# Optimization experiments

Measured on AMD Instinct MI355X. Metric: run time of the kernel, lower is better.

Reference implementation:

```python
import jax, jax.numpy as jnp
import numpy as np

B, L, P = 65536, 512, 96
E_LIN, E = 14, 16
FFT = 512
TEMP = 0.07
K = 2
EPS = 1e-5


def setup_inputs() -> dict:
    key = jax.random.key(0)
    k0, k1, k2 = jax.random.split(key, 3)
    x = jax.random.normal(k0, (B, L), dtype=jnp.float32)
    Wg = jax.random.normal(k1, (E, FFT // 2), dtype=jnp.float32) * 0.02
    bg = jnp.zeros((E,), dtype=jnp.float32)
    Wr = jax.random.normal(k2, (E_LIN, P, L), dtype=jnp.float32) * 0.02
    br = jnp.zeros((E_LIN, P), dtype=jnp.float32)
    return {"x": x, "Wg": Wg, "bg": bg, "Wr": Wr, "br": br}


def _periodogram(x):
    # x: [B, L] -> normalized power spectrum [B, FFT//2]
    x0 = x - jnp.mean(x, axis=1, keepdims=True)
    dft = jnp.fft.fft(x0, n=FFT, axis=1) / np.float32(np.sqrt(FFT))
    dft = dft[:, : FFT // 2]
    I = dft.real ** 2 + dft.imag ** 2
    s = jnp.sum(I, axis=1, keepdims=True)
    s = jnp.where(s == 0, jnp.ones_like(s), s)
    return I / s


def reference(x, Wg, bg, Wr, br):
    # gating (eval mode: no noise, divide by temperature)
    I = _periodogram(x)                                  # [B, F/2]
    gate = (I @ Wg.T + bg) / TEMP                        # [B, E]
    topv, topi = jax.lax.top_k(gate, K)                  # [B, K]
    gates = jax.nn.softmax(topv, axis=1)                 # [B, K]

    # RLinear experts: RevIN(norm) -> Linear -> RevIN(denorm); stats detached
    mu = jax.lax.stop_gradient(jnp.mean(x, axis=1, keepdims=True))        # [B,1]
    sd = jax.lax.stop_gradient(jnp.sqrt(jnp.var(x, axis=1, keepdims=True) + EPS))
    xn = (x - mu) / sd                                   # [B, L]
    yr = jnp.einsum('bl,epl->bep', xn, Wr) + br          # [B, E_LIN, P]
    yr = yr * sd[:, :, None] + mu[:, :, None]

    mean_out = jnp.broadcast_to(jnp.mean(x, axis=1, keepdims=True), (x.shape[0], P))[:, None, :]
    naive_out = jnp.broadcast_to(x[:, -1:], (x.shape[0], P))[:, None, :]

    eo = jnp.concatenate([yr, mean_out, naive_out], axis=1)   # [B, E, P]
    sel = jnp.take_along_axis(eo, topi[:, :, None], axis=1)   # [B, K, P]
    out = jnp.sum(gates[:, :, None] * sel, axis=1)            # [B, P]
    return out
```

## Files before the change

kernel.cpp:

```cpp
#include <hip/hip_runtime.h>
#include <math.h>

#define NB_B 65536
#define NL   512
#define NP   96
#define NE   16
#define NEL  14
#define NF   256
#define TEMP_INV (1.0f/0.07f)
#define TAU  1e-5f
#define PI_D 3.14159265358979323846
#define MAXCHK 1280

typedef __attribute__((ext_vector_type(8))) short bf16x8;
typedef __attribute__((ext_vector_type(4))) float f32x4;


#define WS_PCNT     0
#define WS_PTK      16384
#define WS_PBASE    32768
#define WS_FLAGCNT  33792
#define WS_NCHK     33824
#define WS_FLAG     33856
#define WS_SSUM     296000
#define WS_WGT      301376
#define WS_BGT      317760
#define WS_TWF      317824
#define WS_TWD      319872
#define WS_REC      328064
#define WS_HDR      590208
#define WS_RIDX     1638784
#define WS_WRB      1900928
#define WS_DESC     3473792
#define WS_XB16     3480064

__device__ __forceinline__ unsigned short f2bf(float f) {
    unsigned u = __float_as_uint(f);
    unsigned r = (u + 0x7fffu + ((u >> 16) & 1u)) >> 16;
    return (unsigned short)r;
}

__global__ __launch_bounds__(256) void k_prep(
    const float* __restrict__ Wg, const float* __restrict__ bg,
    const float* __restrict__ Wr,
    float* __restrict__ Ssum, float* __restrict__ WgE, float* __restrict__ bgT,
    double2* __restrict__ twd,
    int* __restrict__ pcnt, int* __restrict__ flagcnt,
    ushort4* __restrict__ Wrb, int perm)
{
    int g = blockIdx.x * 256 + threadIdx.x;
    {
        ushort4 o = make_ushort4(0, 0, 0, 0);
        if (g < NEL * NP * NL / 4) {
            float4 v;
            if (perm) {
                int row = g >> 7, sq = g & 127;
                int ll = sq >> 1, kb = (sq & 1) * 4;
                const float* wr = Wr + (size_t)row * NL + ll;
                v.x = wr[(kb + 0) * 64]; v.y = wr[(kb + 1) * 64];
                v.z = wr[(kb + 2) * 64]; v.w = wr[(kb + 3) * 64];
            } else {
                v = ((const float4*)Wr)[g];
            }
            o.x = f2bf(v.x); o.y = f2bf(v.y); o.z = f2bf(v.z); o.w = f2bf(v.w);
        }
        Wrb[g] = o;
    }
    if (g < NEL * NP) {
        const float4* w = (const float4*)(Wr + (size_t)g * NL);
        float s = 0.f;
        for (int i = 0; i < NL / 4; i++) { float4 v = w[i]; s += v.x + v.y + v.z + v.w; }
        Ssum[g] = s;
    }
    if (g < 4096) {
        int c = g & 3, e = (g >> 2) & 15, f4 = g >> 6;
        WgE[g] = Wg[e * NF + f4 * 4 + c] * TEMP_INV;
    }
    if (g < 512) {
        double a = -2.0 * PI_D * (double)g / 512.0;
        twd[g] = make_double2(cos(a), sin(a));
    }
    if (g < 256) pcnt[g << 4] = 0;
    if (g < NE) bgT[g] = bg[g] * TEMP_INV;
    if (g == 300) *flagcnt = 0;
}

__global__ __launch_bounds__(256) void k_gate(
    const float* __restrict__ x,
    const float4* __restrict__ WgE4, const float* __restrict__ bgT,
    int* __restrict__ rec, float4* __restrict__ hdr,
    int* __restrict__ flaglist, int* __restrict__ flagcnt,
    int* __restrict__ pcnt, unsigned short* __restrict__ xb16)
{
    __shared__ __align__(16) float2 s_z[4][576];
    float* s_Iv = (float*)&s_z[0][0];

    const int t = threadIdx.x;
    const int wv = t >> 6, l = t & 63;
    const int b0 = blockIdx.x * 8 + wv * 2;

    const float kAng = -6.283185307179586f / 512.0f;
    auto mktw = [&](int g) {
        float s_, c_;
        __sincosf((float)g * kAng, &s_, &c_);
        return make_float2(c_, s_);
    };
    float2 tw0[4], tw1[2];
#pragma unroll
    for (int k = 0; k < 4; k++) tw0[k] = mktw(k * 64 + l);
    tw1[0] = mktw(2 * l);
    tw1[1] = mktw(128 + 2 * l);
    const float2 w2 = mktw(l << 2);
    float2 wst[5];
    wst[0] = mktw((l & 31) << 3);
    wst[1] = mktw((l & 15) << 4);
    wst[2] = mktw((l & 7) << 5);
    wst[3] = mktw((l & 3) << 6);
    wst[4] = mktw((l & 1) << 7);

    const float* xa = x + (size_t)b0 * NL;
    const float* xb = xa + NL;
    float xr[8], xi[8];
#pragma unroll
    for (int k = 0; k < 8; k++) { xr[k] = xa[k * 64 + l]; xi[k] = xb[k * 64 + l]; }
    const float last_a = __shfl(xr[7], 63);
    const float last_b = __shfl(xi[7], 63);

    if (xb16) {
        unsigned pa_[4], pb_[4];
#pragma unroll
        for (int j = 0; j < 4; j++) {
            asm("v_cvt_pk_bf16_f32 %0, %1, %2" : "=v"(pa_[j]) : "v"(xr[2 * j]), "v"(xr[2 * j + 1]));
            asm("v_cvt_pk_bf16_f32 %0, %1, %2" : "=v"(pb_[j]) : "v"(xi[2 * j]), "v"(xi[2 * j + 1]));
        }
        *(uint4*)(xb16 + (size_t)b0 * NL + l * 8)       = *(uint4*)pa_;
        *(uint4*)(xb16 + (size_t)(b0 + 1) * NL + l * 8) = *(uint4*)pb_;
    }

#pragma unroll
    for (int k = 0; k < 4; k++) {
        float2 w = tw0[k];
        float ur = xr[k], ui = xi[k], vr = xr[k + 4], vi = xi[k + 4];
        xr[k] = ur + vr; xi[k] = ui + vi;
        float dr = ur - vr, di = ui - vi;
        xr[k + 4] = dr * w.x - di * w.y; xi[k + 4] = dr * w.y + di * w.x;
    }
    {
        const int kk[4] = {0, 1, 4, 5};
#pragma unroll
        for (int g2 = 0; g2 < 4; g2++) {
            int k = kk[g2];
            float2 w = tw1[k & 1];
            float ur = xr[k], ui = xi[k], vr = xr[k + 2], vi = xi[k + 2];
            xr[k] = ur + vr; xi[k] = ui + vi;
            float dr = ur - vr, di = ui - vi;
            xr[k + 2] = dr * w.x - di * w.y; xi[k + 2] = dr * w.y + di * w.x;
        }
    }
    {
#pragma unroll
        for (int k = 0; k < 8; k += 2) {
            float ur = xr[k], ui = xi[k], vr = xr[k + 1], vi = xi[k + 1];
            xr[k] = ur + vr; xi[k] = ui + vi;
            float dr = ur - vr, di = ui - vi;
            xr[k + 1] = dr * w2.x - di * w2.y; xi[k + 1] = dr * w2.y + di * w2.x;
        }
    }
#pragma unroll
    for (int st = 3; st < 8; st++) {
        const int half = 256 >> st;
        const float2 w = wst[st - 3];
        const bool up = (l & half) != 0;
        const float sg = up ? -1.f : 1.f;
        const float cc = up ? w.x : 1.f;
        const float ss = up ? w.y : 0.f;
#pragma unroll
        for (int k = 0; k < 8; k++) {
            float pr = __shfl_xor(xr[k], half);
            float pi = __shfl_xor(xi[k], half);
            float tr = fmaf(sg, xr[k], pr);
            float ti = fmaf(sg, xi[k], pi);
            xr[k] = tr * cc - ti * ss;
            xi[k] = tr * ss + ti * cc;
        }
    }
    {
        const float sg = (l & 1) ? -1.f : 1.f;
#pragma unroll
        for (int k = 0; k < 8; k++) {
            float pr = __shfl_xor(xr[k], 1);
            float pi = __shfl_xor(xi[k], 1);
            xr[k] = fmaf(sg, xr[k], pr);
            xi[k] = fmaf(sg, xi[k], pi);
        }
    }

#pragma unroll
    for (int k = 0; k < 8; k++) {
        int i = k * 64 + l;
        s_z[wv][i + (i >> 3)] = make_float2(xr[k], xi[k]);
    }

    float Ia[4], Ib[4];
    float psa = 0.f, psb = 0.f;
#pragma unroll
    for (int j = 0; j < 4; j++) {
        int f = (l << 2) | j;
        int i1_ = (int)(__brev((unsigned)f) >> 23);
        int i2_ = (int)(__brev((unsigned)((512 - f) & 511)) >> 23);
        float2 z1 = s_z[wv][i1_ + (i1_ >> 3)];
        float2 z2 = s_z[wv][i2_ + (i2_ >> 3)];
        float pr_ = z1.x + z2.x, qm = z1.y - z2.y;
        float qp = z1.y + z2.y, pm = z1.x - z2.x;
        float va = pr_ * pr_ + qm * qm;
        float vb = qp * qp + pm * pm;
        if (f == 0) { va = 0.f; vb = 0.f; }
        Ia[j] = va; Ib[j] = vb;
        psa += va; psb += vb;
    }
#pragma unroll
    for (int m = 1; m < 64; m <<= 1) {
        psa += __shfl_xor(psa, m); psb += __shfl_xor(psb, m);
    }
    const float psa_raw = psa, psb_raw = psb;
    if (psa == 0.f) psa = 1.f;
    if (psb == 0.f) psb = 1.f;
    const float inv_a = 1.f / psa, inv_b = 1.f / psb;

    const float2 Z0   = s_z[wv][0];
    const float2 Z256 = s_z[wv][1];

    float* wI = s_Iv + wv * 1152;
    const int io = (l << 2) + ((l >> 4) << 2);
    *(float4*)(wI + io)       = make_float4(Ia[0], Ia[1], Ia[2], Ia[3]);
    *(float4*)(wI + 272 + io) = make_float4(Ib[0], Ib[1], Ib[2], Ib[3]);

    const int e16 = l & 15, cq = l >> 4;
    const float bgv = bgT[e16];
    float accA = 0.f, accB = 0.f;
    const float* rA = wI + cq * 68;
    const float* rB = rA + 272;
#pragma unroll 4
    for (int jj = 0; jj < 16; jj++) {
        float4 ia = *(const float4*)(rA + 4 * jj);
        float4 ib = *(const float4*)(rB + 4 * jj);
        float4 w = WgE4[(cq * 16 + jj) * 16 + e16];
        accA += ia.x * w.x + ia.y * w.y + ia.z * w.z + ia.w * w.w;
        accB += ib.x * w.x + ib.y * w.y + ib.z * w.z + ib.w * w.w;
    }
    accA += __shfl_xor(accA, 16); accA += __shfl_xor(accA, 32);
    accB += __shfl_xor(accB, 16); accB += __shfl_xor(accB, 32);

    float v = ((l & 16) ? accB * inv_b : accA * inv_a) + bgv;

    float b0v = v; int b0i = e16;
#pragma unroll
    for (int m = 1; m < 16; m <<= 1) {
        float ov = __shfl_xor(b0v, m); int oi = __shfl_xor(b0i, m);
        if (ov > b0v || (ov == b0v && oi < b0i)) { b0v = ov; b0i = oi; }
    }
    float v1 = (e16 == b0i) ? -1e30f : v;
    float b1v = v1; int b1i = e16;
#pragma unroll
    for (int m = 1; m < 16; m <<= 1) {
        float ov = __shfl_xor(b1v, m); int oi = __shfl_xor(b1i, m);
        if (ov > b1v || (ov == b1v && oi < b1i)) { b1v = ov; b1i = oi; }
    }
    float v2 = (e16 == b1i) ? -1e30f : v1;
    float b2v = v2;
#pragma unroll
    for (int m = 1; m < 16; m <<= 1) {
        float ov = __shfl_xor(b2v, m);
        b2v = fmaxf(b2v, ov);
    }

    if (l == 0 || l == 16) {
        const int r = l >> 4;
        const int b = b0 + r;
        const float mu = (r ? Z0.y : Z0.x) * (1.f / 512.f);
        const float Jv = r ? Z256.y : Z256.x;
        const float ps = r ? psb_raw : psa_raw;
        const float sd = sqrtf((0.5f * ps + Jv * Jv) * (1.f / 262144.f) + 1e-5f);
        const float last = r ? last_b : last_a;
        const float w0 = 1.f / (1.f + expf(b1v - b0v));
        const int pid = b0i * 16 + b1i;
        rec[b] = pid;
        hdr[b] = make_float4(mu, sd, last, w0);
        atomicAdd(&pcnt[pid << 4], 1);
        if (b1v - b2v < TAU) {
            int pos = atomicAdd(flagcnt, 1);
            flaglist[pos] = b;
        }
    }
}

__global__ __launch_bounds__(256) void k_refine(
    const float* __restrict__ x, const double2* __restrict__ twd,
    const float* __restrict__ Wg, const float* __restrict__ bg,
    int* __restrict__ rec, float4* __restrict__ hdr,
    const int* __restrict__ flaglist, const int* __restrict__ flagcnt,
    int* __restrict__ pcnt)
{
    __shared__ double s_x[512];
    __shared__ double s_I[256];
    __shared__ double s_red[16];
    __shared__ double s_g[16];
    const int nf = *flagcnt;
    const int t = threadIdx.x;
    const int wid = t >> 6, lane = t & 63;
    for (int fi = blockIdx.x; fi < nf; fi += gridDim.x) {
        const int b = flaglist[fi];
        const float* xp = x + (size_t)b * NL;
        double v0 = (double)xp[t], v1 = (double)xp[t + 256];
        double lsum = v0 + v1;
        for (int m = 1; m < 64; m <<= 1) lsum += __shfl_xor(lsum, m);
        if (lane == 0) s_red[wid] = lsum;
        __syncthreads();
        double mu = (s_red[0] + s_red[1] + s_red[2] + s_red[3]) * (1.0 / 512.0);
        s_x[t] = v0 - mu; s_x[t + 256] = v1 - mu;
        __syncthreads();
        double2 w = twd[t];
        double pr = 1.0, pi = 0.0, cr = 0.0, ci = 0.0;
        for (int n = 0; n < 512; n++) {
            double xv = s_x[n];
            cr += xv * pr; ci += xv * pi;
            double t2 = pr * w.x - pi * w.y;
            pi = pr * w.y + pi * w.x;
            pr = t2;
        }
        double I = cr * cr + ci * ci;
        s_I[t] = I;
        double ls = I;
        for (int m = 1; m < 64; m <<= 1) ls += __shfl_xor(ls, m);
        if (lane == 0) s_red[8 + wid] = ls;
        __syncthreads();
        double stot = s_red[8] + s_red[9] + s_red[10] + s_red[11];
        if (stot == 0.0) stot = 1.0;
        if (t < 16) {
            double acc = 0.0;
            const float* wrow = Wg + t * NF;
            for (int f = 0; f < NF; f++) acc += s_I[f] * (double)wrow[f];
            s_g[t] = (acc / stot + (double)bg[t]) * (1.0 / 0.07);
        }
        __syncthreads();
        if (t == 0) {
            double c0 = -1e300, c1 = -1e300; int j0 = 0, j1 = 0;
            for (int i = 0; i < 16; i++) {
                double v = s_g[i];
                if (v > c0) { c1 = c0; j1 = j0; c0 = v; j0 = i; }
                else if (v > c1) { c1 = v; j1 = i; }
            }
            double e1 = exp(c1 - c0);
            float w0f = (float)(1.0 / (1.0 + e1));
            int newpid = j0 * 16 + j1;
            int old = rec[b];
            if (newpid != old) {
                atomicSub(&pcnt[old << 4], 1);
                atomicAdd(&pcnt[newpid << 4], 1);
                rec[b] = newpid;
            }
            ((float*)(hdr + b))[3] = w0f;
        }
        __syncthreads();
    }
}

__global__ __launch_bounds__(256) void k_scan(
    const int* __restrict__ pcnt, int* __restrict__ pbase, int* __restrict__ ptk,
    int* __restrict__ desc, int* __restrict__ nchk)
{
    __shared__ int s[256], c[256];
    const int t = threadIdx.x;
    const int n = pcnt[t << 4];
    s[t] = n;
    c[t] = (n + 63) >> 6;
    __syncthreads();
    for (int off = 1; off < 256; off <<= 1) {
        int v1 = (t >= off) ? s[t - off] : 0;
        int v2 = (t >= off) ? c[t - off] : 0;
        __syncthreads();
        s[t] += v1; c[t] += v2;
        __syncthreads();
    }
    int excl = t ? s[t - 1] : 0;
    int cexcl = t ? c[t - 1] : 0;
    pbase[t] = excl;
    ptk[t << 4] = excl;
    int myc = (n + 63) >> 6;
    for (int j = 0; j < myc; j++) desc[cexcl + j] = (t << 16) | j;
    if (t == 255) *nchk = cexcl + myc;
}

__global__ __launch_bounds__(256) void k_scatter(
    const int* __restrict__ rec, int* __restrict__ ptk, int* __restrict__ ridx)
{
    __shared__ int h[256], base_[256];
    const int t = threadIdx.x;
    const int b = blockIdx.x * 256 + t;
    h[t] = 0;
    __syncthreads();
    int pid = rec[b];
    int lo = atomicAdd(&h[pid], 1);
    __syncthreads();
    if (h[t]) base_[t] = atomicAdd(&ptk[t << 4], h[t]);
    __syncthreads();
    ridx[base_[pid] + lo] = b;
}

template<int XB>
__global__ __launch_bounds__(256) void k_gemm(
    const float* __restrict__ x, const unsigned short* __restrict__ xb16,
    const unsigned short* __restrict__ Wrb,
    const float* __restrict__ br, const float* __restrict__ Ssum,
    const float4* __restrict__ hdr, float* __restrict__ out,
    const int* __restrict__ pcnt, const int* __restrict__ pbase,
    const int* __restrict__ ridx,
    const int* __restrict__ desc, const int* __restrict__ nchk)
{
    __shared__ __align__(16) unsigned short sA[64 * 72];
    __shared__ __align__(16) unsigned short sB[2][96 * 72];
    __shared__ int    s_idx[64];
    __shared__ float4 s_hdr[64];
    __shared__ float  s_br[2][96], s_S[2][96];
    if ((int)blockIdx.x >= *nchk) return;
    const int d = desc[blockIdx.x];
    const int pid = d >> 16, cc = d & 0xffff;
    const int n = pcnt[pid << 4];
    const int base = pbase[pid];
    const int i0 = pid >> 4, i1 = pid & 15;
    const int t = threadIdx.x;
    const int lane = t & 63, wv = t >> 6;
    const int quad = lane >> 4, l16 = lane & 15;
    const int ar = t >> 2, asub = t & 3;
    if (t < 96) {
        s_br[0][t] = (i0 < NEL) ? br[i0 * NP + t] : 0.f;
        s_S [0][t] = (i0 < NEL) ? Ssum[i0 * NP + t] : 0.f;
        s_br[1][t] = (i1 < NEL) ? br[i1 * NP + t] : 0.f;
        s_S [1][t] = (i1 < NEL) ? Ssum[i1 * NP + t] : 0.f;
    }
    if (t < 64) {
        int g = cc * 64 + t;
        bool vld = g < n;
        int row = vld ? ridx[base + g] : -1;
        s_idx[t] = row;
        s_hdr[t] = vld ? hdr[row] : make_float4(0.f, 0.f, 0.f, 0.f);
    }
    __syncthreads();

    f32x4 acc[2][6];
#pragma unroll
    for (int ex = 0; ex < 2; ex++)
#pragma unroll
        for (int j = 0; j < 6; j++) acc[ex][j] = (f32x4){0.f, 0.f, 0.f, 0.f};

    int rr = s_idx[ar]; if (rr < 0) rr = s_idx[0];

    unsigned boff[6];
    unsigned short* bdst[6];
    const unsigned short* wb[2];
    wb[0] = Wrb + (size_t)i0 * NP * NL;
    wb[1] = Wrb + (size_t)i1 * NP * NL;
    int bex[6];
#pragma unroll
    for (int it = 0; it < 6; it++) {
        int ex = (it >= 3);
        int fl = t + (it - 3 * ex) * 256;
        int p = fl >> 3, kg = fl & 7;
        bex[it] = ex;
        boff[it] = (unsigned)(p * NL + kg * 8);
        bdst[it] = &sB[ex][p * 72 + kg * 8];
    }
    unsigned short* adst = sA + ar * 72 + asub * 16;

    const unsigned short* xrow16 = xb16 + (size_t)rr * NL + asub * 16;
    const float* xrowf = x + (size_t)rr * NL + asub * 16;

    bf16x8 aR[2]; float4 fA[4]; bf16x8 bR[6];

    if constexpr (XB) {
        aR[0] = *(const bf16x8*)(xrow16);
        aR[1] = *(const bf16x8*)(xrow16 + 8);
    } else {
#pragma unroll
        for (int i = 0; i < 4; i++) fA[i] = ((const float4*)xrowf)[i];
    }
#pragma unroll
    for (int it = 0; it < 6; it++) bR[it] = *(const bf16x8*)(wb[bex[it]] + boff[it]);

    for (int kb = 0; kb < NL; kb += 64) {
        if constexpr (XB) {
            *(bf16x8*)adst       = aR[0];
            *(bf16x8*)(adst + 8) = aR[1];
        } else {
            unsigned short tmp[16];
#pragma unroll
            for (int i = 0; i < 4; i++) {
                float4 v = fA[i];
                tmp[i * 4 + 0] = f2bf(v.x); tmp[i * 4 + 1] = f2bf(v.y);
                tmp[i * 4 + 2] = f2bf(v.z); tmp[i * 4 + 3] = f2bf(v.w);
            }
            *(bf16x8*)adst       = *(bf16x8*)tmp;
            *(bf16x8*)(adst + 8) = *(bf16x8*)(tmp + 8);
        }
#pragma unroll
        for (int it = 0; it < 6; it++) *(bf16x8*)bdst[it] = bR[it];
        __syncthreads();

        const int kn = kb + 64;
        if (kn < NL) {
            if constexpr (XB) {
                aR[0] = *(const bf16x8*)(xrow16 + kn);
                aR[1] = *(const bf16x8*)(xrow16 + kn + 8);
            } else {
#pragma unroll
                for (int i = 0; i < 4; i++) fA[i] = ((const float4*)(xrowf + kn))[i];
            }
#pragma unroll
            for (int it = 0; it < 6; it++)
                bR[it] = *(const bf16x8*)(wb[bex[it]] + boff[it] + kn);
        }

#pragma unroll
        for (int ks = 0; ks < 2; ks++) {
            bf16x8 af = *(const bf16x8*)(sA + (wv * 16 + l16) * 72 + ks * 32 + quad * 8);
#pragma unroll
            for (int ex = 0; ex < 2; ex++)
#pragma unroll
                for (int nt = 0; nt < 6; nt++) {
                    bf16x8 bf = *(const bf16x8*)(&sB[ex][(nt * 16 + l16) * 72 + ks * 32 + quad * 8]);
                    acc[ex][nt] = __builtin_amdgcn_mfma_f32_16x16x32_bf16(af, bf, acc[ex][nt], 0, 0, 0);
                }
        }
        __syncthreads();
    }
#pragma unroll
    for (int i = 0; i < 4; i++) {
        int rloc = wv * 16 + quad * 4 + i;
        int row = s_idx[rloc];
        if (row >= 0) {
            float4 h = s_hdr[rloc];
            float mu = h.x, sd = h.y, last = h.z, w0 = h.w, w1 = 1.f - w0;
            float* orow = out + (size_t)row * NP;
#pragma unroll
            for (int nt = 0; nt < 6; nt++) {
                int p = nt * 16 + l16;
                float v0 = (i0 < NEL) ? (mu + s_br[0][p] * sd - mu * s_S[0][p] + acc[0][nt][i])
                                      : (i0 == NEL ? mu : last);
                float v1 = (i1 < NEL) ? (mu + s_br[1][p] * sd - mu * s_S[1][p] + acc[1][nt][i])
                                      : (i1 == NEL ? mu : last);
                orow[p] = w0 * v0 + w1 * v1;
            }
        }
    }
}

extern "C" void kernel_launch(void* const* d_in, const int* in_sizes, int n_in,
                              void* d_out, int out_size, void* d_ws, size_t ws_size,
                              hipStream_t stream)
{
    const float* x  = (const float*)d_in[0];
    const float* Wg = (const float*)d_in[1];
    const float* bg = (const float*)d_in[2];
    const float* Wr = (const float*)d_in[3];
    const float* br = (const float*)d_in[4];
    float* out = (float*)d_out;
    char* ws = (char*)d_ws;

    int*     pcnt     = (int*)(ws + WS_PCNT);
    int*     ptk      = (int*)(ws + WS_PTK);
    int*     pbase    = (int*)(ws + WS_PBASE);
    int*     flagcnt  = (int*)(ws + WS_FLAGCNT);
    int*     nchk     = (int*)(ws + WS_NCHK);
    int*     flaglist = (int*)(ws + WS_FLAG);
    float*   Ssum     = (float*)(ws + WS_SSUM);
    float*   WgE      = (float*)(ws + WS_WGT);
    float*   bgT      = (float*)(ws + WS_BGT);
    double2* twd      = (double2*)(ws + WS_TWD);
    int*     rec      = (int*)(ws + WS_REC);
    float4*  hdr      = (float4*)(ws + WS_HDR);
    int*     ridx     = (int*)(ws + WS_RIDX);
    unsigned short* Wrb = (unsigned short*)(ws + WS_WRB);
    int*     desc     = (int*)(ws + WS_DESC);

    const size_t xb_bytes = (size_t)NB_B * NL * 2;
    const int use_xb = (ws_size >= (size_t)WS_XB16 + xb_bytes);
    unsigned short* xb16 = use_xb ? (unsigned short*)(ws + WS_XB16) : (unsigned short*)0;

    k_prep<<<dim3(768), dim3(256), 0, stream>>>(Wg, bg, Wr, Ssum, WgE, bgT, twd,
                                                pcnt, flagcnt, (ushort4*)Wrb, use_xb);
    k_gate<<<dim3(NB_B / 8), dim3(256), 0, stream>>>(x, (const float4*)WgE, bgT,
                                                     rec, hdr, flaglist, flagcnt, pcnt, xb16);
    k_refine<<<dim3(512), dim3(256), 0, stream>>>(x, twd, Wg, bg, rec, hdr,
                                                  flaglist, flagcnt, pcnt);
    k_scan<<<dim3(1), dim3(256), 0, stream>>>(pcnt, pbase, ptk, desc, nchk);
    k_scatter<<<dim3(NB_B / 256), dim3(256), 0, stream>>>(rec, ptk, ridx);
    if (use_xb)
        k_gemm<1><<<dim3(MAXCHK), dim3(256), 0, stream>>>(x, xb16, Wrb, br, Ssum, hdr, out,
                                                          pcnt, pbase, ridx, desc, nchk);
    else
        k_gemm<0><<<dim3(MAXCHK), dim3(256), 0, stream>>>(x, xb16, Wrb, br, Ssum, hdr, out,
                                                          pcnt, pbase, ridx, desc, nchk);
}
```

Measured before the change: 310.8 us.

## Assign bucket slots during gating and simplify scatter using hole markers

The gating kernel now takes each row's slot within its expert-pair bucket from the count atomic and packs it into rec. The scatter kernel then becomes a direct write with no shared-memory histogram or global atomics. Rows whose pair changes during refinement get a new slot, and their old slot is marked -1, which the GEMM skips. MAXCHK is raised to cover the extra chunks this can create. Separately, Ssum computation is spread over 8 lanes per row, and twiddle factor generation uses fewer sincos calls by exploiting symmetry.

Measured after the change: 296.7 us. -4.5%, faster.

```diff
diff --git a/kernel.cpp b/kernel.cpp
--- a/kernel.cpp
+++ b/kernel.cpp
@@ -10,22 +10,22 @@
 #define TEMP_INV (1.0f/0.07f)
 #define TAU  1e-5f
 #define PI_D 3.14159265358979323846
-#define MAXCHK 1280
+#define MAXCHK 1536
 
 typedef __attribute__((ext_vector_type(8))) short bf16x8;
 typedef __attribute__((ext_vector_type(4))) float f32x4;
 
 
 #define WS_PCNT     0
-#define WS_PTK      16384
+#define WS_HOLES    16384
 #define WS_PBASE    32768
 #define WS_FLAGCNT  33792
 #define WS_NCHK     33824
+#define WS_HOLECNT  33840
 #define WS_FLAG     33856
 #define WS_SSUM     296000
 #define WS_WGT      301376
 #define WS_BGT      317760
-#define WS_TWF      317824
 #define WS_TWD      319872
 #define WS_REC      328064
 #define WS_HDR      590208
@@ -45,7 +45,7 @@
     const float* __restrict__ Wr,
     float* __restrict__ Ssum, float* __restrict__ WgE, float* __restrict__ bgT,
     double2* __restrict__ twd,
-    int* __restrict__ pcnt, int* __restrict__ flagcnt,
+    int* __restrict__ pcnt, int* __restrict__ flagcnt, int* __restrict__ holecnt,
     ushort4* __restrict__ Wrb, int perm)
 {
     int g = blockIdx.x * 256 + threadIdx.x;
@@ -66,11 +66,14 @@
         }
         Wrb[g] = o;
     }
-    if (g < NEL * NP) {
-        const float4* w = (const float4*)(Wr + (size_t)g * NL);
+    if (g < NEL * NP * 8) {
+        int row = g >> 3, seg = g & 7;
+        const float4* w = (const float4*)(Wr + (size_t)row * NL + seg * 64);
         float s = 0.f;
-        for (int i = 0; i < NL / 4; i++) { float4 v = w[i]; s += v.x + v.y + v.z + v.w; }
-        Ssum[g] = s;
+#pragma unroll
+        for (int i = 0; i < 16; i++) { float4 v = w[i]; s += v.x + v.y + v.z + v.w; }
+        s += __shfl_xor(s, 1); s += __shfl_xor(s, 2); s += __shfl_xor(s, 4);
+        if (seg == 0) Ssum[row] = s;
     }
     if (g < 4096) {
         int c = g & 3, e = (g >> 2) & 15, f4 = g >> 6;
@@ -83,6 +86,7 @@
     if (g < 256) pcnt[g << 4] = 0;
     if (g < NE) bgT[g] = bg[g] * TEMP_INV;
     if (g == 300) *flagcnt = 0;
+    if (g == 301) *holecnt = 0;
 }
 
 __global__ __launch_bounds__(256) void k_gate(
@@ -99,24 +103,33 @@
     const int wv = t >> 6, l = t & 63;
     const int b0 = blockIdx.x * 8 + wv * 2;
 
-    const float kAng = -6.283185307179586f / 512.0f;
-    auto mktw = [&](int g) {
-        float s_, c_;
-        __sincosf((float)g * kAng, &s_, &c_);
-        return make_float2(c_, s_);
-    };
-    float2 tw0[4], tw1[2];
-#pragma unroll
-    for (int k = 0; k < 4; k++) tw0[k] = mktw(k * 64 + l);
-    tw1[0] = mktw(2 * l);
-    tw1[1] = mktw(128 + 2 * l);
-    const float2 w2 = mktw(l << 2);
+    const float th = -6.283185307179586f / 512.0f;
+    const float R2 = 0.70710678118654752f;
+    float s1, c1; __sincosf((float)l * th, &s1, &c1);
+    float s2, c2; __sincosf((float)(2 * l) * th, &s2, &c2);
+    float sw0, cw0; __sincosf((float)((l & 31) << 3) * th, &sw0, &cw0);
+    float sw1, cw1; __sincosf((float)((l & 15) << 4) * th, &sw1, &cw1);
+    float sw2, cw2; __sincosf((float)((l & 7) << 5) * th, &sw2, &cw2);
+    float2 tw0[4];
+    tw0[0] = make_float2(c1, s1);
+    tw0[1] = make_float2(R2 * (c1 + s1), R2 * (s1 - c1));
+    tw0[2] = make_float2(s1, -c1);
+    tw0[3] = make_float2(tw0[1].y, -tw0[1].x);
+    float2 tw1[2];
+    tw1[0] = make_float2(c2, s2);
+    tw1[1] = make_float2(s2, -c2);
+    const float2 w2 = make_float2(c2 * c2 - s2 * s2, 2.f * c2 * s2);
     float2 wst[5];
-    wst[0] = mktw((l & 31) << 3);
-    wst[1] = mktw((l & 15) << 4);
-    wst[2] = mktw((l & 7) << 5);
-    wst[3] = mktw((l & 3) << 6);
-    wst[4] = mktw((l & 1) << 7);
+    wst[0] = make_float2(cw0, sw0);
+    wst[1] = make_float2(cw1, sw1);
+    wst[2] = make_float2(cw2, sw2);
+    {
+        int j2 = l & 3;
+        float cc3 = (j2 == 0) ? 1.f : (j2 == 1) ? R2 : (j2 == 2) ? 0.f : -R2;
+        float ss3 = (j2 == 0) ? 0.f : (j2 == 2) ? -1.f : -R2;
+        wst[3] = make_float2(cc3, ss3);
+    }
+    wst[4] = (l & 1) ? make_float2(0.f, -1.f) : make_float2(1.f, 0.f);
 
     const float* xa = x + (size_t)b0 * NL;
     const float* xb = xa + NL;
@@ -284,9 +297,9 @@
         const float last = r ? last_b : last_a;
         const float w0 = 1.f / (1.f + expf(b1v - b0v));
         const int pid = b0i * 16 + b1i;
-        rec[b] = pid;
+        const int lo = atomicAdd(&pcnt[pid << 4], 1);
+        rec[b] = (pid << 24) | lo;
         hdr[b] = make_float4(mu, sd, last, w0);
-        atomicAdd(&pcnt[pid << 4], 1);
         if (b1v - b2v < TAU) {
             int pos = atomicAdd(flagcnt, 1);
             flaglist[pos] = b;
@@ -299,7 +312,7 @@
     const float* __restrict__ Wg, const float* __restrict__ bg,
     int* __restrict__ rec, float4* __restrict__ hdr,
     const int* __restrict__ flaglist, const int* __restrict__ flagcnt,
-    int* __restrict__ pcnt)
+    int* __restrict__ pcnt, int* __restrict__ holes, int* __restrict__ holecnt)
 {
     __shared__ double s_x[512];
     __shared__ double s_I[256];
@@ -353,20 +366,26 @@
             double e1 = exp(c1 - c0);
             float w0f = (float)(1.0 / (1.0 + e1));
             int newpid = j0 * 16 + j1;
-            int old = rec[b];
-            if (newpid != old) {
-                atomicSub(&pcnt[old << 4], 1);
-                atomicAdd(&pcnt[newpid << 4], 1);
-                rec[b] = newpid;
+            int oldrec = rec[b];
+            int oldpid = (int)(((unsigned)oldrec) >> 24);
+            if (newpid == oldpid) {
+                ((float*)(hdr + b))[3] = w0f;
+            } else {
+                int pos = atomicAdd(holecnt, 1);
+                if (pos < 4096) {
+                    int nlo = atomicAdd(&pcnt[newpid << 4], 1);
+                    rec[b] = (newpid << 24) | nlo;
+                    holes[pos] = oldrec;
+                    ((float*)(hdr + b))[3] = w0f;
+                }
             }
-            ((float*)(hdr + b))[3] = w0f;
         }
         __syncthreads();
     }
 }
 
 __global__ __launch_bounds__(256) void k_scan(
-    const int* __restrict__ pcnt, int* __restrict__ pbase, int* __restrict__ ptk,
+    const int* __restrict__ pcnt, int* __restrict__ pbase,
     int* __restrict__ desc, int* __restrict__ nchk)
 {
     __shared__ int s[256], c[256];
@@ -385,26 +404,27 @@
     int excl = t ? s[t - 1] : 0;
     int cexcl = t ? c[t - 1] : 0;
     pbase[t] = excl;
-    ptk[t << 4] = excl;
     int myc = (n + 63) >> 6;
     for (int j = 0; j < myc; j++) desc[cexcl + j] = (t << 16) | j;
     if (t == 255) *nchk = cexcl + myc;
 }
 
 __global__ __launch_bounds__(256) void k_scatter(
-    const int* __restrict__ rec, int* __restrict__ ptk, int* __restrict__ ridx)
+    const int* __restrict__ rec, const int* __restrict__ pbase,
+    int* __restrict__ ridx,
+    const int* __restrict__ holes, const int* __restrict__ holecnt)
 {
-    __shared__ int h[256], base_[256];
     const int t = threadIdx.x;
     const int b = blockIdx.x * 256 + t;
-    h[t] = 0;
-    __syncthreads();
-    int pid = rec[b];
-    int lo = atomicAdd(&h[pid], 1);
-    __syncthreads();
-    if (h[t]) base_[t] = atomicAdd(&ptk[t << 4], h[t]);
-    __syncthreads();
-    ridx[base_[pid] + lo] = b;
+    unsigned v = (unsigned)rec[b];
+    ridx[pbase[v >> 24] + (v & 0xFFFFFF)] = b;
+    if (blockIdx.x == 0) {
+        int nh = *holecnt; if (nh > 4096) nh = 4096;
+        for (int h = t; h < nh; h += 256) {
+            unsigned hv = (unsigned)holes[h];
+            ridx[pbase[hv >> 24] + (hv & 0xFFFFFF)] = -1;
+        }
+    }
 }
 
 template<int XB>
@@ -443,7 +463,7 @@
         bool vld = g < n;
         int row = vld ? ridx[base + g] : -1;
         s_idx[t] = row;
-        s_hdr[t] = vld ? hdr[row] : make_float4(0.f, 0.f, 0.f, 0.f);
+        s_hdr[t] = (row >= 0) ? hdr[row] : make_float4(0.f, 0.f, 0.f, 0.f);
     }
     __syncthreads();
 
@@ -453,7 +473,7 @@
 #pragma unroll
         for (int j = 0; j < 6; j++) acc[ex][j] = (f32x4){0.f, 0.f, 0.f, 0.f};
 
-    int rr = s_idx[ar]; if (rr < 0) rr = s_idx[0];
+    int rr = s_idx[ar]; if (rr < 0) rr = 0;
 
     unsigned boff[6];
     unsigned short* bdst[6];
@@ -567,10 +587,11 @@
     char* ws = (char*)d_ws;
 
     int*     pcnt     = (int*)(ws + WS_PCNT);
-    int*     ptk      = (int*)(ws + WS_PTK);
+    int*     holes    = (int*)(ws + WS_HOLES);
     int*     pbase    = (int*)(ws + WS_PBASE);
     int*     flagcnt  = (int*)(ws + WS_FLAGCNT);
     int*     nchk     = (int*)(ws + WS_NCHK);
+    int*     holecnt  = (int*)(ws + WS_HOLECNT);
     int*     flaglist = (int*)(ws + WS_FLAG);
     float*   Ssum     = (float*)(ws + WS_SSUM);
     float*   WgE      = (float*)(ws + WS_WGT);
@@ -587,13 +608,14 @@
     unsigned short* xb16 = use_xb ? (unsigned short*)(ws + WS_XB16) : (unsigned short*)0;
 
     k_prep<<<dim3(768), dim3(256), 0, stream>>>(Wg, bg, Wr, Ssum, WgE, bgT, twd,
-                                                pcnt, flagcnt, (ushort4*)Wrb, use_xb);
+                                                pcnt, flagcnt, holecnt,
+                                                (ushort4*)Wrb, use_xb);
     k_gate<<<dim3(NB_B / 8), dim3(256), 0, stream>>>(x, (const float4*)WgE, bgT,
                                                      rec, hdr, flaglist, flagcnt, pcnt, xb16);
     k_refine<<<dim3(512), dim3(256), 0, stream>>>(x, twd, Wg, bg, rec, hdr,
-                                                  flaglist, flagcnt, pcnt);
-    k_scan<<<dim3(1), dim3(256), 0, stream>>>(pcnt, pbase, ptk, desc, nchk);
-    k_scatter<<<dim3(NB_B / 256), dim3(256), 0, stream>>>(rec, ptk, ridx);
+                                                  flaglist, flagcnt, pcnt, holes, holecnt);
+    k_scan<<<dim3(1), dim3(256), 0, stream>>>(pcnt, pbase, desc, nchk);
+    k_scatter<<<dim3(NB_B / 256), dim3(256), 0, stream>>>(rec, pbase, ridx, holes, holecnt);
     if (use_xb)
         k_gemm<1><<<dim3(MAXCHK), dim3(256), 0, stream>>>(x, xb16, Wrb, br, Ssum, hdr, out,
                                                           pcnt, pbase, ridx, desc, nchk);
```
